# Performance work log

Hardware: AMD Instinct MI355X
Metric: run time of the kernel (lower is better)

## Reference

```python
import jax, jax.numpy as jnp
import numpy as np

B, J, C = 4096, 17, 512       # batch, joints (length), channels (dim)
K, TOK, CH, H, KS, G = 3, 64, 1024, 8, 3, 8  # adj kernels, tokens_dim, channels_dim, heads, conv_large, gn groups
EPS = 1e-5


def setup_inputs() -> dict:
    key = jax.random.key(0)
    ks = jax.random.split(key, 16)
    r = lambda i, shp, s=0.02: jax.random.normal(ks[i], shp, jnp.float32) * s
    return {
        "x": jax.random.normal(ks[0], (B, J, C), jnp.float32),
        "adj": jax.random.uniform(ks[1], (K, J, J), jnp.float32) / J,
        "norm1_w": jnp.ones((J,), jnp.float32), "norm1_b": jnp.zeros((J,), jnp.float32),
        "gcn1_w": r(2, (K * C, C)), "gcn1_b": jnp.zeros((K * C,), jnp.float32),
        "dw_w": r(3, (C, 1, KS), 0.1), "dw_b": jnp.zeros((C,), jnp.float32),
        "gn1_w": jnp.ones((C,), jnp.float32), "gn1_b": jnp.zeros((C,), jnp.float32),
        "pw_w": r(4, (C, C)), "pw_b": jnp.zeros((C,), jnp.float32),
        "mlp1_w1": r(5, (TOK, J)), "mlp1_b1": jnp.zeros((TOK,), jnp.float32),
        "mlp1_w2": r(6, (J, TOK)), "mlp1_b2": jnp.zeros((J,), jnp.float32),
        "qkv_w": r(7, (3 * C, C)), "qkv_b": jnp.zeros((3 * C,), jnp.float32),
        "proj_w": r(8, (C, C)), "proj_b": jnp.zeros((C,), jnp.float32),
        "gnf_w": jnp.ones((C,), jnp.float32), "gnf_b": jnp.zeros((C,), jnp.float32),
        "norm2_w": jnp.ones((C,), jnp.float32), "norm2_b": jnp.zeros((C,), jnp.float32),
        "mlp2_w1": r(9, (CH, C)), "mlp2_b1": jnp.zeros((CH,), jnp.float32),
        "mlp2_w2": r(10, (C, CH)), "mlp2_b2": jnp.zeros((C,), jnp.float32),
        "gcn2_w": r(11, (K * C, C)), "gcn2_b": jnp.zeros((K * C,), jnp.float32),
    }


def _gelu(t):
    return jax.nn.gelu(t, approximate=False)  # torch nn.GELU default is exact erf


def _ln(t, w, b):  # LayerNorm over last axis
    m = t.mean(-1, keepdims=True)
    v = ((t - m) ** 2).mean(-1, keepdims=True)
    return (t - m) * jax.lax.rsqrt(v + EPS) * w + b


def _gn(t, w, b):  # GroupNorm(G, C) over (B, C, J)
    Bn, Cc, Jn = t.shape
    r = t.reshape(Bn, G, -1)
    m = r.mean(-1, keepdims=True)
    v = ((r - m) ** 2).mean(-1, keepdims=True)
    r = (r - m) * jax.lax.rsqrt(v + EPS)
    return r.reshape(Bn, Cc, Jn) * w[:, None] + b[:, None]


def _gcn(t, w, b, adj):  # t: (B,C,J); 1x1 conv to K*C then einsum with adj (K,J,J)
    y = jnp.einsum('bcj,oc->boj', t, w) + b[:, None]
    y = y.reshape(t.shape[0], K, C, t.shape[2])
    return jnp.einsum('bkcv,kvw->bcw', y, adj)


def reference(x, adj, norm1_w, norm1_b, gcn1_w, gcn1_b, dw_w, dw_b, gn1_w, gn1_b,
              pw_w, pw_b, mlp1_w1, mlp1_b1, mlp1_w2, mlp1_b2, qkv_w, qkv_b,
              proj_w, proj_b, gnf_w, gnf_b, norm2_w, norm2_b,
              mlp2_w1, mlp2_b1, mlp2_w2, mlp2_b2, gcn2_w, gcn2_b):
    res = x                                   # (B,J,C)
    xc = jnp.swapaxes(x, 1, 2)                # (B,C,J)
    xc = _ln(xc, norm1_w, norm1_b)            # LayerNorm over joints

    # --- branch 1: GCN ---
    x_gcn1 = _gcn(xc, gcn1_w, gcn1_b, adj)    # (B,C,J)

    # --- branch 2: depthwise conv + token MLP ---
    h = jax.lax.conv_general_dilated(xc, dw_w, (1,), [(KS // 2, KS // 2)],
                                     dimension_numbers=('NCH', 'OIH', 'NCH'),
                                     feature_group_count=C) + dw_b[:, None]
    h = _gelu(_gn(h, gn1_w, gn1_b))
    h = jnp.einsum('bcj,oc->boj', h, pw_w) + pw_b[:, None]      # 1x1 conv
    h = _gelu(jnp.einsum('bcj,tj->bct', h, mlp1_w1) + mlp1_b1)  # token mlp fc1
    h = jnp.einsum('bct,jt->bcj', h, mlp1_w2) + mlp1_b2         # token mlp fc2

    # --- branch 3: global spatial attention over joints ---
    dh = C // H
    qkv = jnp.einsum('bcj,oc->boj', xc, qkv_w) + qkv_b[:, None]  # (B,3C,J)
    q, k_, v_ = jnp.split(qkv, 3, axis=1)
    q = q.reshape(-1, H, dh, J); k_ = k_.reshape(-1, H, dh, J); v_ = v_.reshape(-1, H, dh, J)
    attn = jax.nn.softmax(jnp.einsum('bhdi,bhdj->bhij', q, k_) / jnp.sqrt(jnp.float32(dh)), axis=-1)
    sga = jnp.einsum('bhij,bhdj->bhdi', attn, v_).reshape(-1, C, J)
    sga = jnp.einsum('bcj,oc->boj', sga, proj_w) + proj_b[:, None]

    # --- fuse ---
    xc = _gelu(_gn(sga + x_gcn1 + h, gnf_w, gnf_b))
    xj = jnp.swapaxes(xc, 1, 2)               # (B,J,C)
    res_channel = xj
    xn = _ln(xj + res, norm2_w, norm2_b)      # LayerNorm over channels
    m = _gelu(jnp.einsum('bjc,hc->bjh', xn, mlp2_w1) + mlp2_b1)
    m = jnp.einsum('bjh,ch->bjc', m, mlp2_w2) + mlp2_b2
    g2 = _gcn(jnp.swapaxes(m, 1, 2), gcn2_w, gcn2_b, adj)  # (B,C,J)
    xj = res_channel + jnp.swapaxes(g2, 1, 2)
    return xj + res
```

## Files before the change

kernel.cpp:

```cpp
#include <hip/hip_runtime.h>
#include <stdint.h>

#define BB 4096
#define JJ 17
#define CC 512

typedef unsigned short u16;
typedef __bf16 bf16x8 __attribute__((ext_vector_type(8)));
typedef float  f32x4  __attribute__((ext_vector_type(4)));

__device__ __forceinline__ float bf2f(u16 u){ return __uint_as_float(((uint32_t)u)<<16); }
__device__ __forceinline__ u16 f2bf(float f){
  uint32_t u = __float_as_uint(f);
  u += 0x7fffu + ((u>>16)&1u);
  return (u16)(u>>16);
}
__device__ __forceinline__ void unpk2(uint32_t u, float& lo, float& hi){
  lo = __uint_as_float(u<<16);
  hi = __uint_as_float(u & 0xffff0000u);
}
__device__ __forceinline__ float gelu_f(float x){
  float x2 = x*x;
  float y2 = x*fmaf(0.0713548162726f, x2, 1.59576912161f);
  float ey = __builtin_amdgcn_exp2f(y2*1.44269504089f);
  return fmaf(-x, __builtin_amdgcn_rcpf(ey+1.f), x);
}
__device__ __forceinline__ void gll16(const void* g, void* l){
  __builtin_amdgcn_global_load_lds(
      (const __attribute__((address_space(1))) void*)g,
      (__attribute__((address_space(3))) void*)l, 16, 0, 0);
}

__global__ void k_cvt7(const float* __restrict__ s0,const float* __restrict__ s1,
                       const float* __restrict__ s2,const float* __restrict__ s3,
                       const float* __restrict__ s4,const float* __restrict__ s5,
                       const float* __restrict__ s6, u16* __restrict__ out){
  int i = blockIdx.x*blockDim.x + threadIdx.x;
  if (i >= 3932160) return;
  const float* src; int off;
  if      (i < 786432)  { src=s0; off=0; }
  else if (i < 1572864) { src=s1; off=786432; }
  else if (i < 1835008) { src=s2; off=1572864; }
  else if (i < 2097152) { src=s3; off=1835008; }
  else if (i < 2621440) { src=s4; off=2097152; }
  else if (i < 3145728) { src=s5; off=2621440; }
  else                  { src=s6; off=3145728; }
  out[i] = f2bf(src[i-off]);
}

__global__ void k_tokprep(const float* __restrict__ w1, const float* __restrict__ w2,
                          u16* __restrict__ w1m, u16* __restrict__ w2m){
  int i = blockIdx.x*blockDim.x + threadIdx.x;
  if (i < 2560){ int t=i/40, j=i%40; w1m[i] = (j<17) ? f2bf(w1[t*17+j]) : (u16)0; }
  int k = i - 2560;
  if (k >= 0 && k < 2304){ int j=k/72, t=k%72; w2m[k] = (j<17 && t<64) ? f2bf(w2[j*64+t]) : (u16)0; }
}

__global__ __launch_bounds__(512) void k_pre(
    const float* __restrict__ x, int b0,
    const float* __restrict__ n1w, const float* __restrict__ n1b,
    const float* __restrict__ dww, const float* __restrict__ dwb,
    const float* __restrict__ gn1w, const float* __restrict__ gn1b,
    u16* __restrict__ xc, u16* __restrict__ hgn)
{
  int b = blockIdx.x, c = threadIdx.x;
  const float* xp = x + (size_t)(b0+b)*JJ*CC + c;
  float v[JJ]; float s = 0.f;
  #pragma unroll
  for (int j=0;j<JJ;j++){ v[j] = xp[(size_t)j*CC]; s += v[j]; }
  float mn = s*(1.f/JJ); float var = 0.f;
  #pragma unroll
  for (int j=0;j<JJ;j++){ float d=v[j]-mn; var += d*d; }
  float rr = rsqrtf(var*(1.f/JJ)+1e-5f);
  float xcv[JJ];
  #pragma unroll
  for (int j=0;j<JJ;j++) xcv[j] = (v[j]-mn)*rr*n1w[j] + n1b[j];
  u16* xo = xc + (size_t)b*JJ*CC + c;
  #pragma unroll
  for (int j=0;j<JJ;j++) xo[(size_t)j*CC] = f2bf(xcv[j]);
  float w0=dww[c*3+0], w1=dww[c*3+1], w2=dww[c*3+2], db=dwb[c];
  float h[JJ];
  #pragma unroll
  for (int j=0;j<JJ;j++){
    float a = db + w1*xcv[j];
    if (j>0)    a += w0*xcv[j-1];
    if (j<JJ-1) a += w2*xcv[j+1];
    h[j] = a;
  }
  float ss=0.f, sq=0.f;
  #pragma unroll
  for (int j=0;j<JJ;j++){ ss += h[j]; sq += h[j]*h[j]; }
  for (int off=32; off; off>>=1){ ss += __shfl_xor(ss,off); sq += __shfl_xor(sq,off); }
  float gm = ss*(1.f/(64.f*JJ));
  float gr = rsqrtf(sq*(1.f/(64.f*JJ)) - gm*gm + 1e-5f);
  float gw = gn1w[c], gb = gn1b[c];
  u16* ho = hgn + (size_t)b*JJ*CC + c;
  #pragma unroll
  for (int j=0;j<JJ;j++){
    float t = (h[j]-gm)*gr*gw + gb;
    ho[(size_t)j*CC] = f2bf(gelu_f(t));
  }
}

template<int DO_GELU, int DO_ADD>
__global__ __launch_bounds__(512,4) void gemm_r5(
    const u16* __restrict__ A, const u16* __restrict__ W, const float* __restrict__ bias,
    u16* __restrict__ out, const u16* __restrict__ add0, const u16* __restrict__ add1,
    int M, int N, int K, int NXT)
{
  __shared__ __align__(16) u16 lds[36864];
  const int tid = threadIdx.x;
  const int wid = tid>>6, lane = tid&63;

  const int nwg = gridDim.x;
  const int q8 = nwg>>3, r8 = nwg&7;
  const int xcd = blockIdx.x & 7, sub = blockIdx.x >> 3;
  const int wg = (xcd<r8 ? xcd*(q8+1) : r8*(q8+1)+(xcd-r8)*q8) + sub;
  const int n0 = (wg % NXT)*256;
  const int m0 = (wg / NXT)*128;

  const int wm = wid>>2, wn = wid&3;
  const int lr = lane&15, lg = lane>>4;
  const int T  = K>>5;

  const int agsw = ((tid&3) ^ ((tid>>3)&3))<<3;
  const u16* gA  = A + (size_t)(m0 + (tid>>2))*K + agsw;
  const u16* gB0 = W + (size_t)(n0 + (tid>>2))*K + agsw;
  const u16* gB1 = W + (size_t)(n0 + 128 + (tid>>2))*K + agsw;
  const int dstl = tid*8;

  const int g8 = (lg ^ ((lr>>1)&3))<<3;
  const int offA0 = (wm*64+lr)*32 + g8;
  const int offB0 = 4096 + (wn*64+lr)*32 + g8;

  f32x4 acc[4][4];
  #pragma unroll
  for (int i=0;i<4;i++)
    #pragma unroll
    for (int j=0;j<4;j++) acc[i][j] = (f32x4){0.f,0.f,0.f,0.f};

  auto STAGE = [&](int t, int sofs){
    gll16(gA  + t*32, lds + sofs + dstl);
    gll16(gB0 + t*32, lds + sofs + 4096 + dstl);
    gll16(gB1 + t*32, lds + sofs + 8192 + dstl);
  };

  STAGE(0, 0); STAGE(1, 12288);
  asm volatile("s_waitcnt vmcnt(3)" ::: "memory");
  __builtin_amdgcn_s_barrier();

  int s0 = 0, s1 = 12288, s2 = 24576;
  for (int t=0; t<T; ++t){
    const bool more = (t+2 < T);
    if (more) STAGE(t+2, s2);
    bf16x8 av[4], bv[4];
    #pragma unroll
    for (int i=0;i<4;i++) av[i] = *(const bf16x8*)&lds[s0 + offA0 + i*512];
    #pragma unroll
    for (int j=0;j<4;j++) bv[j] = *(const bf16x8*)&lds[s0 + offB0 + j*512];
    __builtin_amdgcn_s_setprio(1);
    #pragma unroll
    for (int i=0;i<4;i++)
      #pragma unroll
      for (int j=0;j<4;j++)
        acc[i][j] = __builtin_amdgcn_mfma_f32_16x16x32_bf16(av[i], bv[j], acc[i][j], 0,0,0);
    __builtin_amdgcn_s_setprio(0);
    if (more) asm volatile("s_waitcnt vmcnt(3)" ::: "memory");
    else      asm volatile("s_waitcnt vmcnt(0)" ::: "memory");
    __builtin_amdgcn_s_barrier();
    const int tmp = s0; s0 = s1; s1 = s2; s2 = tmp;
  }

  const int rbase = lg*4;
  #pragma unroll
  for (int i=0;i<4;i++){
    #pragma unroll
    for (int j=0;j<4;j++){
      const int col  = n0 + wn*64 + j*16 + lr;
      const int row0 = m0 + wm*64 + i*16 + rbase;
      const float bvl = bias[col];
      #pragma unroll
      for (int r=0;r<4;r++){
        size_t idx = (size_t)(row0+r)*N + col;
        float v = acc[i][j][r] + bvl;
        if (DO_ADD)  v += bf2f(add0[idx]) + bf2f(add1[idx]);
        if (DO_GELU) v = gelu_f(v);
        out[idx] = f2bf(v);
      }
    }
  }
}

template<int FINAL>
__global__ __launch_bounds__(512) void k_gcn2(
    const u16* __restrict__ G, const float* __restrict__ adj,
    u16* __restrict__ xg,
    const u16* __restrict__ tsum, int b0,
    float* __restrict__ out)
{
  __shared__ __align__(16) float adjp[51*20];
  const int tid = threadIdx.x;
  for (int i=tid; i<1020; i+=512){
    int r=i/20, cl=i%20;
    adjp[i] = (cl<17) ? adj[r*17+cl] : 0.f;
  }
  __syncthreads();

  const int sl  = tid>>7;
  const int l   = tid&127;
  const int c0  = l*4;
  const int bl  = blockIdx.x*4 + sl;

  float acc[JJ][4];
  #pragma unroll
  for (int w=0;w<JJ;w++)
    #pragma unroll
    for (int e=0;e<4;e++) acc[w][e]=0.f;

  const u16* gbase = G + (size_t)bl*JJ*1536 + c0;
  #pragma unroll 3
  for (int kv=0; kv<51; kv++){
    const int k = kv/JJ, v = kv - k*JJ;
    uint2 yu = *(const uint2*)(gbase + (size_t)v*1536 + k*512);
    float y0,y1,y2,y3;
    unpk2(yu.x, y0, y1);
    unpk2(yu.y, y2, y3);
    const f32x4* arow = (const f32x4*)&adjp[kv*20];
    f32x4 a0=arow[0], a1=arow[1], a2=arow[2], a3=arow[3];
    float a16 = adjp[kv*20+16];
    float ar[JJ] = {a0[0],a0[1],a0[2],a0[3], a1[0],a1[1],a1[2],a1[3],
                    a2[0],a2[1],a2[2],a2[3], a3[0],a3[1],a3[2],a3[3], a16};
    #pragma unroll
    for (int w=0;w<JJ;w++){
      acc[w][0] += y0*ar[w];
      acc[w][1] += y1*ar[w];
      acc[w][2] += y2*ar[w];
      acc[w][3] += y3*ar[w];
    }
  }

  if (FINAL==0){
    u16* xo = xg + (size_t)bl*JJ*CC + c0;
    #pragma unroll
    for (int w=0;w<JJ;w++){
      uint2 o;
      o.x = (uint32_t)f2bf(acc[w][0]) | ((uint32_t)f2bf(acc[w][1])<<16);
      o.y = (uint32_t)f2bf(acc[w][2]) | ((uint32_t)f2bf(acc[w][3])<<16);
      *(uint2*)(xo + (size_t)w*CC) = o;
    }
  } else {
    const size_t lb = (size_t)bl*JJ*CC + c0;
    const size_t gb = (size_t)(b0+bl)*JJ*CC + c0;
    #pragma unroll
    for (int w=0;w<JJ;w++){
      uint2 tu = *(const uint2*)(tsum + lb + (size_t)w*CC);
      float t0,t1,t2,t3;
      unpk2(tu.x, t0, t1);
      unpk2(tu.y, t2, t3);
      f32x4 o;
      o[0]=acc[w][0]+t0; o[1]=acc[w][1]+t1;
      o[2]=acc[w][2]+t2; o[3]=acc[w][3]+t3;
      *(f32x4*)(out + gb + (size_t)w*CC) = o;
    }
  }
}

__global__ __launch_bounds__(512) void k_attn(const u16* __restrict__ Gqkv, u16* __restrict__ sga){
  __shared__ __align__(16) u16 qs[8*17*72];
  __shared__ __align__(16) u16 ks_[8*17*72];
  __shared__ __align__(16) float at[8*17*20];
  int b = blockIdx.x, tid = threadIdx.x;
  int h = tid>>6, d = tid&63;
  const u16* base = Gqkv + (size_t)b*JJ*1536;
  float vv[JJ];
  #pragma unroll
  for (int i=0;i<JJ;i++){
    qs [(h*JJ+i)*72 + d] = base[(size_t)i*1536 +        h*64 + d];
    ks_[(h*JJ+i)*72 + d] = base[(size_t)i*1536 +  512 + h*64 + d];
    vv[i] = bf2f(base[(size_t)i*1536 + 1024 + h*64 + d]);
  }
  __syncthreads();
  for (int p=d; p<289; p+=64){
    int i=p/JJ, j=p-i*JJ;
    const u16* qrow = &qs [(h*JJ+i)*72];
    const u16* krow = &ks_[(h*JJ+j)*72];
    float a=0.f;
    #pragma unroll
    for (int t=0;t<8;t++){
      bf16x8 q8 = *(const bf16x8*)&qrow[t*8];
      bf16x8 k8 = *(const bf16x8*)&krow[t*8];
      #pragma unroll
      for (int e=0;e<8;e++) a += (float)q8[e]*(float)k8[e];
    }
    at[(h*JJ+i)*20 + j] = a*0.125f;
  }
  __syncthreads();
  if (d < JJ){
    float* row = &at[(h*JJ+d)*20];
    f32x4 r0=((f32x4*)row)[0], r1=((f32x4*)row)[1], r2=((f32x4*)row)[2], r3=((f32x4*)row)[3];
    float e16=row[16];
    float rv[JJ]={r0[0],r0[1],r0[2],r0[3],r1[0],r1[1],r1[2],r1[3],
                  r2[0],r2[1],r2[2],r2[3],r3[0],r3[1],r3[2],r3[3],e16};
    float mx=-1e30f;
    #pragma unroll
    for (int j=0;j<JJ;j++) mx=fmaxf(mx,rv[j]);
    float sm=0.f;
    #pragma unroll
    for (int j=0;j<JJ;j++){ rv[j]=__builtin_amdgcn_exp2f((rv[j]-mx)*1.44269504089f); sm+=rv[j]; }
    float inv=1.f/sm;
    #pragma unroll
    for (int j=0;j<JJ;j++) row[j]=rv[j]*inv;
  }
  __syncthreads();
  #pragma unroll
  for (int i=0;i<JJ;i++){
    const float* row = &at[(h*JJ+i)*20];
    f32x4 r0=((const f32x4*)row)[0], r1=((const f32x4*)row)[1],
          r2=((const f32x4*)row)[2], r3=((const f32x4*)row)[3];
    float a = r0[0]*vv[0]+r0[1]*vv[1]+r0[2]*vv[2]+r0[3]*vv[3]
            + r1[0]*vv[4]+r1[1]*vv[5]+r1[2]*vv[6]+r1[3]*vv[7]
            + r2[0]*vv[8]+r2[1]*vv[9]+r2[2]*vv[10]+r2[3]*vv[11]
            + r3[0]*vv[12]+r3[1]*vv[13]+r3[2]*vv[14]+r3[3]*vv[15]
            + row[16]*vv[16];
    sga[((size_t)b*JJ+i)*CC + h*64 + d] = f2bf(a);
  }
}

__global__ __launch_bounds__(256) void k_tok(const u16* __restrict__ Hpw,
    const u16* __restrict__ w1m, const u16* __restrict__ w2m,
    const float* __restrict__ b1, const float* __restrict__ b2,
    u16* __restrict__ h2o){
  __shared__ __align__(16) u16 lds[31488];
  __shared__ float b1s[64], b2s[32];
  const int tid = threadIdx.x, wid = tid>>6, lane = tid&63;
  const int lr = lane&15, lg = lane>>4;
  const int bl = blockIdx.x;
  const f32x4 zz = {0.f,0.f,0.f,0.f};

  for (int i=tid; i<2560; i+=256) lds[26624+i] = w1m[i];
  for (int i=tid; i<2304; i+=256) lds[29184+i] = w2m[i];
  if (tid<64) b1s[tid] = b1[tid];
  if (tid<32) b2s[tid] = (tid<17) ? b2[tid] : 0.f;
  {
    const int base = tid*40;
    lds[base+17]=0; lds[base+18]=0; lds[base+19]=0;
    #pragma unroll
    for (int q=0;q<5;q++) *(uint2*)&lds[base+20+q*4] = (uint2){0u,0u};
  }
  __syncthreads();

  const u16* hp = Hpw + (size_t)bl*JJ*CC;
  u16* op = h2o + (size_t)bl*JJ*CC;

  for (int pass=0; pass<2; ++pass){
    const int cbase = pass*256;
    for (int idx=tid; idx<1088; idx+=256){
      int j = idx>>6, cq = (idx&63)<<2;
      uint2 u = *(const uint2*)(hp + (size_t)j*CC + cbase + cq);
      lds[(cq  )*40 + j] = (u16)(u.x & 0xffffu);
      lds[(cq+1)*40 + j] = (u16)(u.x >> 16);
      lds[(cq+2)*40 + j] = (u16)(u.y & 0xffffu);
      lds[(cq+3)*40 + j] = (u16)(u.y >> 16);
    }
    __syncthreads();

    bf16x8 av1[4];
    #pragma unroll
    for (int mt=0;mt<4;mt++) av1[mt] = *(const bf16x8*)&lds[26624 + (mt*16+lr)*40 + lg*8];
    #pragma unroll
    for (int nt=0;nt<4;nt++){
      const int cl = wid*64 + nt*16 + lr;
      bf16x8 bv = *(const bf16x8*)&lds[cl*40 + lg*8];
      #pragma unroll
      for (int mt=0;mt<4;mt++){
        f32x4 ac = __builtin_amdgcn_mfma_f32_16x16x32_bf16(av1[mt], bv, zz, 0,0,0);
        const int t0 = mt*16 + lg*4;
        float g0 = gelu_f(ac[0] + b1s[t0+0]);
        float g1 = gelu_f(ac[1] + b1s[t0+1]);
        float g2 = gelu_f(ac[2] + b1s[t0+2]);
        float g3 = gelu_f(ac[3] + b1s[t0+3]);
        uint2 pk;
        pk.x = (uint32_t)f2bf(g0) | ((uint32_t)f2bf(g1)<<16);
        pk.y = (uint32_t)f2bf(g2) | ((uint32_t)f2bf(g3)<<16);
        const int gi = (10240 + cl*64 + t0) ^ ((cl&7)<<3);
        *(uint2*)&lds[gi] = pk;
      }
    }
    asm volatile("s_waitcnt lgkmcnt(0)" ::: "memory");
    __builtin_amdgcn_sched_barrier(0);

    bf16x8 av2[2][2];
    #pragma unroll
    for (int mt=0;mt<2;mt++)
      #pragma unroll
      for (int kt=0;kt<2;kt++)
        av2[mt][kt] = *(const bf16x8*)&lds[29184 + (mt*16+lr)*72 + kt*32 + lg*8];
    #pragma unroll
    for (int nt=0;nt<4;nt++){
      const int cl = wid*64 + nt*16 + lr;
      f32x4 a20 = zz, a21 = zz;
      #pragma unroll
      for (int kt=0;kt<2;kt++){
        const int gi = (10240 + cl*64 + kt*32 + lg*8) ^ ((cl&7)<<3);
        bf16x8 bv2 = *(const bf16x8*)&lds[gi];
        a20 = __builtin_amdgcn_mfma_f32_16x16x32_bf16(av2[0][kt], bv2, a20, 0,0,0);
        a21 = __builtin_amdgcn_mfma_f32_16x16x32_bf16(av2[1][kt], bv2, a21, 0,0,0);
      }
      const int c = cbase + cl;
      #pragma unroll
      for (int r=0;r<4;r++){
        const int j = lg*4 + r;
        op[(size_t)j*CC + c] = f2bf(a20[r] + b2s[j]);
      }
      if (lg==0) op[(size_t)16*CC + c] = f2bf(a21[0] + b2s[16]);
    }
    __syncthreads();
  }
}

__global__ __launch_bounds__(512) void k_fuse_a(const u16* __restrict__ s,
    const float* __restrict__ x, int b0,
    const float* __restrict__ gfw, const float* __restrict__ gfb,
    u16* __restrict__ tsum){
  const int tid = threadIdx.x;
  const int sl  = tid>>7;
  const int l   = tid&127;
  const int c0  = l*4;
  const int bl  = blockIdx.x*4 + sl;

  const u16* sp = s + (size_t)bl*JJ*CC + c0;
  float sv[JJ][4];
  float ss=0.f, sq=0.f;
  #pragma unroll
  for (int j=0;j<JJ;j++){
    uint2 u = *(const uint2*)(sp + (size_t)j*CC);
    unpk2(u.x, sv[j][0], sv[j][1]);
    unpk2(u.y, sv[j][2], sv[j][3]);
    #pragma unroll
    for (int e=0;e<4;e++){ ss += sv[j][e]; sq = fmaf(sv[j][e], sv[j][e], sq); }
  }
  #pragma unroll
  for (int off=8; off; off>>=1){ ss += __shfl_xor(ss,off); sq += __shfl_xor(sq,off); }
  float gm = ss*(1.f/1088.f);
  float gr = rsqrtf(sq*(1.f/1088.f) - gm*gm + 1e-5f);

  f32x4 gw = *(const f32x4*)(gfw + c0);
  f32x4 gb = *(const f32x4*)(gfb + c0);
  const float* xp = x + (size_t)(b0+bl)*JJ*CC + c0;
  u16* tp = tsum + (size_t)bl*JJ*CC + c0;
  #pragma unroll
  for (int j=0;j<JJ;j++){
    f32x4 xv = *(const f32x4*)(xp + (size_t)j*CC);
    float t0 = gelu_f((sv[j][0]-gm)*gr*gw[0] + gb[0]) + xv[0];
    float t1 = gelu_f((sv[j][1]-gm)*gr*gw[1] + gb[1]) + xv[1];
    float t2 = gelu_f((sv[j][2]-gm)*gr*gw[2] + gb[2]) + xv[2];
    float t3 = gelu_f((sv[j][3]-gm)*gr*gw[3] + gb[3]) + xv[3];
    uint2 o;
    o.x = (uint32_t)f2bf(t0) | ((uint32_t)f2bf(t1)<<16);
    o.y = (uint32_t)f2bf(t2) | ((uint32_t)f2bf(t3)<<16);
    *(uint2*)(tp + (size_t)j*CC) = o;
  }
}

__global__ __launch_bounds__(512) void k_ln(const u16* __restrict__ tsum,
    const float* __restrict__ n2w, const float* __restrict__ n2b,
    u16* __restrict__ xn){
  const int wid = threadIdx.x>>6, lane = threadIdx.x&63;
  const size_t tk = (size_t)blockIdx.x*8 + wid;
  const u16* tp = tsum + tk*CC + lane*8;
  uint4 u = *(const uint4*)tp;
  float v[8];
  unpk2(u.x, v[0], v[1]);
  unpk2(u.y, v[2], v[3]);
  unpk2(u.z, v[4], v[5]);
  unpk2(u.w, v[6], v[7]);
  float ss=0.f, sq=0.f;
  #pragma unroll
  for (int e=0;e<8;e++){ ss += v[e]; sq = fmaf(v[e], v[e], sq); }
  #pragma unroll
  for (int off=32; off; off>>=1){ ss += __shfl_xor(ss,off); sq += __shfl_xor(sq,off); }
  float mn = ss*(1.f/512.f);
  float r2 = rsqrtf(sq*(1.f/512.f) - mn*mn + 1e-5f);
  f32x4 w0 = *(const f32x4*)(n2w + lane*8);
  f32x4 w1 = *(const f32x4*)(n2w + lane*8 + 4);
  f32x4 b0 = *(const f32x4*)(n2b + lane*8);
  f32x4 b1 = *(const f32x4*)(n2b + lane*8 + 4);
  float wv[8] = {w0[0],w0[1],w0[2],w0[3], w1[0],w1[1],w1[2],w1[3]};
  float bv[8] = {b0[0],b0[1],b0[2],b0[3], b1[0],b1[1],b1[2],b1[3]};
  u16 o[8];
  #pragma unroll
  for (int e=0;e<8;e++) o[e] = f2bf((v[e]-mn)*r2*wv[e] + bv[e]);
  uint4 pk;
  pk.x = (uint32_t)o[0] | ((uint32_t)o[1]<<16);
  pk.y = (uint32_t)o[2] | ((uint32_t)o[3]<<16);
  pk.z = (uint32_t)o[4] | ((uint32_t)o[5]<<16);
  pk.w = (uint32_t)o[6] | ((uint32_t)o[7]<<16);
  *(uint4*)(xn + tk*CC + lane*8) = pk;
}

extern "C" void kernel_launch(void* const* d_in, const int* in_sizes, int n_in,
                              void* d_out, int out_size, void* d_ws, size_t ws_size,
                              hipStream_t stream)
{
  const float* x      = (const float*)d_in[0];
  const float* adj    = (const float*)d_in[1];
  const float* n1w    = (const float*)d_in[2];
  const float* n1b    = (const float*)d_in[3];
  const float* gcn1_w = (const float*)d_in[4];
  const float* gcn1_b = (const float*)d_in[5];
  const float* dw_w   = (const float*)d_in[6];
  const float* dw_b   = (const float*)d_in[7];
  const float* gn1_w  = (const float*)d_in[8];
  const float* gn1_b  = (const float*)d_in[9];
  const float* pw_w   = (const float*)d_in[10];
  const float* pw_b   = (const float*)d_in[11];
  const float* m1w1   = (const float*)d_in[12];
  const float* m1b1   = (const float*)d_in[13];
  const float* m1w2   = (const float*)d_in[14];
  const float* m1b2   = (const float*)d_in[15];
  const float* qkv_w  = (const float*)d_in[16];
  const float* qkv_b  = (const float*)d_in[17];
  const float* proj_w = (const float*)d_in[18];
  const float* proj_b = (const float*)d_in[19];
  const float* gnf_w  = (const float*)d_in[20];
  const float* gnf_b  = (const float*)d_in[21];
  const float* n2w    = (const float*)d_in[22];
  const float* n2b    = (const float*)d_in[23];
  const float* m2w1   = (const float*)d_in[24];
  const float* m2b1   = (const float*)d_in[25];
  const float* m2w2   = (const float*)d_in[26];
  const float* m2b2   = (const float*)d_in[27];
  const float* gcn2_w = (const float*)d_in[28];
  const float* gcn2_b = (const float*)d_in[29];
  float* out = (float*)d_out;

  char* ws = (char*)d_ws;
  const size_t WBYTES = (size_t)3932160*2;
  const size_t TPBYTES = (2560+2304)*2;

  const int cands[5] = {4096,2048,1024,512,256};
  int NB = 0;
  for (int ci=0; ci<5; ci++){
    size_t need = WBYTES + TPBYTES + (size_t)cands[ci]*JJ*2*(1536 + 4*512);
    if (need <= ws_size){ NB = cands[ci]; break; }
  }
  if (NB == 0) return;

  u16* wb = (u16*)ws;
  u16* w1m = (u16*)(ws + WBYTES);
  u16* w2m = w1m + 2560;
  char* p = ws + WBYTES + TPBYTES;
  const size_t SZ_BIGc = (size_t)NB*JJ*1536*2;
  const size_t SZTc    = (size_t)NB*JJ*512*2;
  u16* big = (u16*)p;               p += SZ_BIGc;
  u16* t0  = (u16*)p;               p += SZTc;
  u16* t1  = (u16*)p;               p += SZTc;
  u16* t2  = (u16*)p;               p += SZTc;
  u16* t3  = (u16*)p;

  u16 *wg1=wb, *wqkv=wb+786432, *wpw=wb+1572864, *wproj=wb+1835008,
      *wm1=wb+2097152, *wm2=wb+2621440, *wg2=wb+3145728;

  k_cvt7<<<(3932160+255)/256,256,0,stream>>>(gcn1_w,qkv_w,pw_w,proj_w,m2w1,m2w2,gcn2_w,wb);
  k_tokprep<<<19,256,0,stream>>>(m1w1,m1w2,w1m,w2m);

  const int M2 = NB*JJ;
  const int MT = M2/128;
  for (int b0 = 0; b0 < BB; b0 += NB){
    k_pre<<<NB,512,0,stream>>>(x,b0,n1w,n1b,dw_w,dw_b,gn1_w,gn1_b, t0, t1);
    gemm_r5<0,0><<<MT*6,512,0,stream>>>(t0,wg1,gcn1_b,big,nullptr,nullptr,M2,1536,512,6);
    k_gcn2<0><<<NB/4,512,0,stream>>>(big,adj,t2,nullptr,0,nullptr);
    gemm_r5<0,0><<<MT*6,512,0,stream>>>(t0,wqkv,qkv_b,big,nullptr,nullptr,M2,1536,512,6);
    k_attn<<<NB,512,0,stream>>>(big,t3);
    gemm_r5<0,0><<<MT*2,512,0,stream>>>(t1,wpw,pw_b,t0,nullptr,nullptr,M2,512,512,2);
    k_tok<<<NB,256,0,stream>>>(t0,w1m,w2m,m1b1,m1b2,t1);
    gemm_r5<0,1><<<MT*2,512,0,stream>>>(t3,wproj,proj_b,t0,t2,t1,M2,512,512,2);
    k_fuse_a<<<NB/4,512,0,stream>>>(t0,x,b0,gnf_w,gnf_b,t3);
    k_ln<<<M2/8,512,0,stream>>>(t3,n2w,n2b,t2);
    gemm_r5<1,0><<<MT*4,512,0,stream>>>(t2,wm1,m2b1,big,nullptr,nullptr,M2,1024,512,4);
    gemm_r5<0,0><<<MT*2,512,0,stream>>>(big,wm2,m2b2,t0,nullptr,nullptr,M2,512,1024,2);
    gemm_r5<0,0><<<MT*6,512,0,stream>>>(t0,wg2,gcn2_b,big,nullptr,nullptr,M2,1536,512,6);
    k_gcn2<1><<<NB/4,512,0,stream>>>(big,adj,nullptr,t3,b0,out);
  }
}
```

Measured before the change: 1.259 ms.

## Rewrite GEMM as 256x256 tile with K=64 steps and interleaved 8-phase pipeline

Replaces the 128x256 GEMM tile, which used a triple-buffered K=32 pipeline, with a 256x256 tile using double-buffered K=64 stages. Each iteration is split into four MFMA quadrants, and the loads for the next stage are interleaved between them behind barriers. The larger tile raises arithmetic intensity and operand reuse per LDS read. In exchange, occupancy drops to 2 workgroups per CU, LDS rises to 128KB, and M2 must be divisible by 256, which may produce fewer workgroups for the smaller GEMMs.

```diff
diff --git a/kernel.cpp b/kernel.cpp
--- a/kernel.cpp
+++ b/kernel.cpp
@@ -103,12 +103,12 @@
 }
 
 template<int DO_GELU, int DO_ADD>
-__global__ __launch_bounds__(512,4) void gemm_r5(
+__global__ __launch_bounds__(512,2) void gemm_8p(
     const u16* __restrict__ A, const u16* __restrict__ W, const float* __restrict__ bias,
     u16* __restrict__ out, const u16* __restrict__ add0, const u16* __restrict__ add1,
     int M, int N, int K, int NXT)
 {
-  __shared__ __align__(16) u16 lds[36864];
+  __shared__ __align__(16) u16 lds[65536];
   const int tid = threadIdx.x;
   const int wid = tid>>6, lane = tid&63;
 
@@ -117,67 +117,135 @@
   const int xcd = blockIdx.x & 7, sub = blockIdx.x >> 3;
   const int wg = (xcd<r8 ? xcd*(q8+1) : r8*(q8+1)+(xcd-r8)*q8) + sub;
   const int n0 = (wg % NXT)*256;
-  const int m0 = (wg / NXT)*128;
+  const int m0 = (wg / NXT)*256;
 
   const int wm = wid>>2, wn = wid&3;
   const int lr = lane&15, lg = lane>>4;
-  const int T  = K>>5;
-
-  const int agsw = ((tid&3) ^ ((tid>>3)&3))<<3;
-  const u16* gA  = A + (size_t)(m0 + (tid>>2))*K + agsw;
-  const u16* gB0 = W + (size_t)(n0 + (tid>>2))*K + agsw;
-  const u16* gB1 = W + (size_t)(n0 + 128 + (tid>>2))*K + agsw;
-  const int dstl = tid*8;
-
-  const int g8 = (lg ^ ((lr>>1)&3))<<3;
-  const int offA0 = (wm*64+lr)*32 + g8;
-  const int offB0 = 4096 + (wn*64+lr)*32 + g8;
-
-  f32x4 acc[4][4];
-  #pragma unroll
-  for (int i=0;i<4;i++)
+  const int T  = K>>6;
+
+  const int srow = tid>>3;
+  const int gs = ((tid&7) ^ (srow&7))<<3;
+  const u16* pA = A + (size_t)(m0 + srow)*K + gs;
+  const u16* pB = W + (size_t)(n0 + srow)*K + gs;
+  const size_t r64K  = (size_t)64*K;
+  const size_t r128K = (size_t)128*K;
+  const int dst = tid*8;
+
+  const int gk0 = ((0+lg) ^ (lr&7))<<3;
+  const int gk1 = ((4+lg) ^ (lr&7))<<3;
+  const int aro = wm*128 + lr;
+  const int bro = wn*64  + lr;
+
+  f32x4 acc[8][4];
+  #pragma unroll
+  for (int i=0;i<8;i++)
     #pragma unroll
     for (int j=0;j<4;j++) acc[i][j] = (f32x4){0.f,0.f,0.f,0.f};
 
-  auto STAGE = [&](int t, int sofs){
-    gll16(gA  + t*32, lds + sofs + dstl);
-    gll16(gB0 + t*32, lds + sofs + 4096 + dstl);
-    gll16(gB1 + t*32, lds + sofs + 8192 + dstl);
+  bf16x8 aA[2][4], bB0[2][2], bB1[2][2];
+
+  auto ST = [&](const u16* p, int t, int du16){
+    gll16(p + t*64,        lds + du16 + dst);
+    gll16(p + r64K + t*64, lds + du16 + 4096 + dst);
   };
 
-  STAGE(0, 0); STAGE(1, 12288);
-  asm volatile("s_waitcnt vmcnt(3)" ::: "memory");
+  ST(pA,        0, 0);
+  ST(pA+r128K,  0, 8192);
+  ST(pB,        0, 16384);
+  ST(pB+r128K,  0, 24576);
+  if (T > 1) ST(pA, 1, 32768);
+  asm volatile("s_waitcnt vmcnt(2)" ::: "memory");
   __builtin_amdgcn_s_barrier();
 
-  int s0 = 0, s1 = 12288, s2 = 24576;
   for (int t=0; t<T; ++t){
-    const bool more = (t+2 < T);
-    if (more) STAGE(t+2, s2);
-    bf16x8 av[4], bv[4];
-    #pragma unroll
-    for (int i=0;i<4;i++) av[i] = *(const bf16x8*)&lds[s0 + offA0 + i*512];
-    #pragma unroll
-    for (int j=0;j<4;j++) bv[j] = *(const bf16x8*)&lds[s0 + offB0 + j*512];
+    const int s = (t&1)<<15, o = s^32768;
+    const bool m1 = (t+1 < T), m2 = (t+2 < T);
+    #pragma unroll
+    for (int i=0;i<4;i++){
+      const int rb = s + (aro + i*16)*64;
+      aA[0][i] = *(const bf16x8*)&lds[rb + gk0];
+      aA[1][i] = *(const bf16x8*)&lds[rb + gk1];
+    }
+    #pragma unroll
+    for (int j=0;j<2;j++){
+      const int rb = s + 16384 + (bro + j*16)*64;
+      bB0[0][j] = *(const bf16x8*)&lds[rb + gk0];
+      bB0[1][j] = *(const bf16x8*)&lds[rb + gk1];
+    }
+    if (m1) ST(pA+r128K, t+1, o+8192);
+    __builtin_amdgcn_s_barrier();
+    asm volatile("s_waitcnt lgkmcnt(0)" ::: "memory");
     __builtin_amdgcn_s_setprio(1);
     #pragma unroll
-    for (int i=0;i<4;i++)
-      #pragma unroll
-      for (int j=0;j<4;j++)
-        acc[i][j] = __builtin_amdgcn_mfma_f32_16x16x32_bf16(av[i], bv[j], acc[i][j], 0,0,0);
+    for (int kk=0;kk<2;kk++)
+      #pragma unroll
+      for (int i=0;i<4;i++)
+        #pragma unroll
+        for (int j=0;j<2;j++)
+          acc[i][j] = __builtin_amdgcn_mfma_f32_16x16x32_bf16(aA[kk][i], bB0[kk][j], acc[i][j], 0,0,0);
     __builtin_amdgcn_s_setprio(0);
-    if (more) asm volatile("s_waitcnt vmcnt(3)" ::: "memory");
-    else      asm volatile("s_waitcnt vmcnt(0)" ::: "memory");
-    __builtin_amdgcn_s_barrier();
-    const int tmp = s0; s0 = s1; s1 = s2; s2 = tmp;
+    __builtin_amdgcn_s_barrier();
+    #pragma unroll
+    for (int j=0;j<2;j++){
+      const int rb = s + 16384 + (bro + (2+j)*16)*64;
+      bB1[0][j] = *(const bf16x8*)&lds[rb + gk0];
+      bB1[1][j] = *(const bf16x8*)&lds[rb + gk1];
+    }
+    if (m1) ST(pB, t+1, o+16384);
+    __builtin_amdgcn_s_barrier();
+    asm volatile("s_waitcnt lgkmcnt(0)" ::: "memory");
+    __builtin_amdgcn_s_setprio(1);
+    #pragma unroll
+    for (int kk=0;kk<2;kk++)
+      #pragma unroll
+      for (int i=0;i<4;i++)
+        #pragma unroll
+        for (int j=0;j<2;j++)
+          acc[i][2+j] = __builtin_amdgcn_mfma_f32_16x16x32_bf16(aA[kk][i], bB1[kk][j], acc[i][2+j], 0,0,0);
+    __builtin_amdgcn_s_setprio(0);
+    __builtin_amdgcn_s_barrier();
+    #pragma unroll
+    for (int i=0;i<4;i++){
+      const int rb = s + (aro + (4+i)*16)*64;
+      aA[0][i] = *(const bf16x8*)&lds[rb + gk0];
+      aA[1][i] = *(const bf16x8*)&lds[rb + gk1];
+    }
+    if (m1) ST(pB+r128K, t+1, o+24576);
+    __builtin_amdgcn_s_barrier();
+    asm volatile("s_waitcnt lgkmcnt(0)" ::: "memory");
+    __builtin_amdgcn_s_setprio(1);
+    #pragma unroll
+    for (int kk=0;kk<2;kk++)
+      #pragma unroll
+      for (int i=0;i<4;i++)
+        #pragma unroll
+        for (int j=0;j<2;j++)
+          acc[4+i][j] = __builtin_amdgcn_mfma_f32_16x16x32_bf16(aA[kk][i], bB0[kk][j], acc[4+i][j], 0,0,0);
+    __builtin_amdgcn_s_setprio(0);
+    __builtin_amdgcn_s_barrier();
+    if (m2) ST(pA, t+2, s);
+    if (m2) asm volatile("s_waitcnt vmcnt(2)" ::: "memory");
+    else    asm volatile("s_waitcnt vmcnt(0)" ::: "memory");
+    __builtin_amdgcn_s_barrier();
+    __builtin_amdgcn_s_setprio(1);
+    #pragma unroll
+    for (int kk=0;kk<2;kk++)
+      #pragma unroll
+      for (int i=0;i<4;i++)
+        #pragma unroll
+        for (int j=0;j<2;j++)
+          acc[4+i][2+j] = __builtin_amdgcn_mfma_f32_16x16x32_bf16(aA[kk][i], bB1[kk][j], acc[4+i][2+j], 0,0,0);
+    __builtin_amdgcn_s_setprio(0);
+    __builtin_amdgcn_s_barrier();
   }
 
   const int rbase = lg*4;
   #pragma unroll
-  for (int i=0;i<4;i++){
+  for (int i=0;i<8;i++){
     #pragma unroll
     for (int j=0;j<4;j++){
       const int col  = n0 + wn*64 + j*16 + lr;
-      const int row0 = m0 + wm*64 + i*16 + rbase;
+      const int row0 = m0 + wm*128 + i*16 + rbase;
       const float bvl = bias[col];
       #pragma unroll
       for (int r=0;r<4;r++){
@@ -565,21 +633,21 @@
   k_tokprep<<<19,256,0,stream>>>(m1w1,m1w2,w1m,w2m);
 
   const int M2 = NB*JJ;
-  const int MT = M2/128;
+  const int MT = M2/256;
   for (int b0 = 0; b0 < BB; b0 += NB){
     k_pre<<<NB,512,0,stream>>>(x,b0,n1w,n1b,dw_w,dw_b,gn1_w,gn1_b, t0, t1);
-    gemm_r5<0,0><<<MT*6,512,0,stream>>>(t0,wg1,gcn1_b,big,nullptr,nullptr,M2,1536,512,6);
+    gemm_8p<0,0><<<MT*6,512,0,stream>>>(t0,wg1,gcn1_b,big,nullptr,nullptr,M2,1536,512,6);
     k_gcn2<0><<<NB/4,512,0,stream>>>(big,adj,t2,nullptr,0,nullptr);
-    gemm_r5<0,0><<<MT*6,512,0,stream>>>(t0,wqkv,qkv_b,big,nullptr,nullptr,M2,1536,512,6);
+    gemm_8p<0,0><<<MT*6,512,0,stream>>>(t0,wqkv,qkv_b,big,nullptr,nullptr,M2,1536,512,6);
     k_attn<<<NB,512,0,stream>>>(big,t3);
-    gemm_r5<0,0><<<MT*2,512,0,stream>>>(t1,wpw,pw_b,t0,nullptr,nullptr,M2,512,512,2);
+    gemm_8p<0,0><<<MT*2,512,0,stream>>>(t1,wpw,pw_b,t0,nullptr,nullptr,M2,512,512,2);
     k_tok<<<NB,256,0,stream>>>(t0,w1m,w2m,m1b1,m1b2,t1);
-    gemm_r5<0,1><<<MT*2,512,0,stream>>>(t3,wproj,proj_b,t0,t2,t1,M2,512,512,2);
+    gemm_8p<0,1><<<MT*2,512,0,stream>>>(t3,wproj,proj_b,t0,t2,t1,M2,512,512,2);
     k_fuse_a<<<NB/4,512,0,stream>>>(t0,x,b0,gnf_w,gnf_b,t3);
     k_ln<<<M2/8,512,0,stream>>>(t3,n2w,n2b,t2);
-    gemm_r5<1,0><<<MT*4,512,0,stream>>>(t2,wm1,m2b1,big,nullptr,nullptr,M2,1024,512,4);
-    gemm_r5<0,0><<<MT*2,512,0,stream>>>(big,wm2,m2b2,t0,nullptr,nullptr,M2,512,1024,2);
-    gemm_r5<0,0><<<MT*6,512,0,stream>>>(t0,wg2,gcn2_b,big,nullptr,nullptr,M2,1536,512,6);
+    gemm_8p<1,0><<<MT*4,512,0,stream>>>(t2,wm1,m2b1,big,nullptr,nullptr,M2,1024,512,4);
+    gemm_8p<0,0><<<MT*2,512,0,stream>>>(big,wm2,m2b2,t0,nullptr,nullptr,M2,512,1024,2);
+    gemm_8p<0,0><<<MT*6,512,0,stream>>>(t0,wg2,gcn2_b,big,nullptr,nullptr,M2,1536,512,6);
     k_gcn2<1><<<NB/4,512,0,stream>>>(big,adj,nullptr,t3,b0,out);
   }
 }
```

Result: slower. 1.338 ms (+6.3%).
